# Optimization experiments

Hardware: AMD Instinct MI355X
Metric: run time of the kernel (lower is better)

The kernel has to match this reference:

```python
import jax, jax.numpy as jnp
import numpy as np

EPS = 1e-5

def mish(x):
    return x * jnp.tanh(jnp.logaddexp(x, 0.0))

def instance_norm(x, gamma, beta):
    # x: (N, C, D, H, W); normalize per (N, C) over spatial dims
    mu = jnp.mean(x, axis=(2, 3, 4), keepdims=True)
    var = jnp.var(x, axis=(2, 3, 4), keepdims=True)
    xh = (x - mu) * jax.lax.rsqrt(var + EPS)
    return xh * gamma[None, :, None, None, None] + beta[None, :, None, None, None]

def conv3d(x, w, stride, padding):
    return jax.lax.conv_general_dilated(
        x, w, window_strides=(stride, stride, stride), padding=padding,
        dimension_numbers=('NCDHW', 'OIDHW', 'NCDHW'))

def pad_k(k, p):
    # center-pad kernel spatial dims up to 5x5x5
    return jnp.pad(k, ((0, 0), (0, 0), (p, p), (p, p), (p, p)))

def mode_conv(x, t, c5, c3, c1, a3, a5, gw, gb, gamma, beta):
    N = x.shape[0]
    Co = c5.shape[0]
    # gate: Linear(num_tasks -> 5*Co), softmax over the 5 experts
    g = jax.nn.softmax((t @ gw.T + gb).reshape(N, 5, Co), axis=1)  # (N,5,Co)
    pool3 = jnp.full((3, 3, 3), 1.0 / 27.0, x.dtype)
    pool5 = jnp.full((5, 5, 5), 1.0 / 125.0, x.dtype)
    experts = jnp.stack([
        c5,                      # conv5x5
        pad_k(c3, 1),            # conv3x3 padded to 5
        pad_k(c1, 2),            # conv1x1 padded to 5
        pad_k(a3 * pool3, 1),    # avg3x3: (Co,Ci,1,1,1)*(3,3,3) broadcast, padded
        a5 * pool5,              # avg5x5
    ], axis=0)                   # (5, Co, Ci, 5, 5, 5)
    # per-sample synthesized kernel
    w = jnp.einsum('eoidhw,neo->noidhw', experts, g)  # (N, Co, Ci, 5,5,5)
    # per-sample conv3d, padding 'same' (training branch of original)
    y = jax.vmap(lambda xi, wi: conv3d(xi[None], wi, 1, 'SAME')[0])(x, w)
    return mish(instance_norm(y, gamma, beta))

def setup_inputs() -> dict:
    key = jax.random.key(0)
    ks = jax.random.split(key, 32)
    N, Ci, Co, T = 2, 32, 64, 10
    D = H = W = 64
    f32 = jnp.float32
    def kconv(k, co, ci, ksz, fan):
        bound = float(np.sqrt(6.0 / ((1.0 + 5.0) * fan)))  # kaiming_uniform a=sqrt(5), fan_out
        return jax.random.uniform(k, (co, ci, ksz, ksz, ksz), f32, -bound, bound)
    inp = {}
    inp['x'] = jax.random.normal(ks[0], (N, Ci, D, H, W), f32)
    inp['t'] = jax.random.normal(ks[1], (N, T), f32)
    def layer(base, ci, co):
        p = {}
        p['conv5'] = kconv(ks[base + 0], co, ci, 5, co * 125)
        p['conv3'] = kconv(ks[base + 1], co, ci, 3, co * 27)
        p['conv1'] = kconv(ks[base + 2], co, ci, 1, co)
        p['avg3'] = kconv(ks[base + 3], co, ci, 1, co)
        p['avg5'] = kconv(ks[base + 4], co, ci, 1, co)
        gb_bound = 1.0 / np.sqrt(T)
        p['gw'] = jax.random.uniform(ks[base + 5], (5 * co, T), f32, -gb_bound, gb_bound)
        p['gb'] = jax.random.uniform(ks[base + 6], (5 * co,), f32, -gb_bound, gb_bound)
        p['gamma'] = jnp.ones((co,), f32)
        p['beta'] = jnp.zeros((co,), f32)
        return p
    for name, v in layer(2, Ci, Co).items():
        inp['l1_' + name] = v
    for name, v in layer(12, Co, Co).items():
        inp['l2_' + name] = v
    dw_bound = float(np.sqrt(1.0 / (Co * 8)))
    inp['down_w'] = jax.random.uniform(ks[25], (Co, Co, 2, 2, 2), f32, -dw_bound, dw_bound)
    inp['down_gamma'] = jnp.ones((Co,), f32)
    inp['down_beta'] = jnp.zeros((Co,), f32)
    return inp

def reference(x, t,
              l1_conv5, l1_conv3, l1_conv1, l1_avg3, l1_avg5, l1_gw, l1_gb, l1_gamma, l1_beta,
              l2_conv5, l2_conv3, l2_conv1, l2_avg3, l2_avg5, l2_gw, l2_gb, l2_gamma, l2_beta,
              down_w, down_gamma, down_beta):
    h = mode_conv(x, t, l1_conv5, l1_conv3, l1_conv1, l1_avg3, l1_avg5, l1_gw, l1_gb, l1_gamma, l1_beta)
    x_skip = mode_conv(h, t, l2_conv5, l2_conv3, l2_conv1, l2_avg3, l2_avg5, l2_gw, l2_gb, l2_gamma, l2_beta)
    y = conv3d(x_skip, down_w, 2, 'VALID')
    y = mish(instance_norm(y, down_gamma, down_beta))
    return (y, x_skip)
```

## Files before the change

kernel.cpp:

```cpp
#include <hip/hip_runtime.h>
#include <cstdint>
#include <cstddef>

constexpr int NB  = 2;
constexpr int CO  = 64;
constexpr int DIM = 64;
constexpr int SP  = DIM * DIM * DIM;
constexpr int NC  = NB * CO;
constexpr int Y_SZ = NB * CO * 32 * 32 * 32;

typedef float f32x4 __attribute__((ext_vector_type(4)));
typedef short s16x8 __attribute__((ext_vector_type(8)));

__device__ __forceinline__ unsigned short f2bf(float f) {
    unsigned int u = __float_as_uint(f);
    unsigned int r = (u + 0x7fffu + ((u >> 16) & 1u)) >> 16;
    return (unsigned short)r;
}
__device__ __forceinline__ float bf2f(unsigned short u) {
    return __uint_as_float((unsigned int)u << 16);
}
__device__ __forceinline__ unsigned int pack2(float a, float b) {
    return (unsigned int)f2bf(a) | ((unsigned int)f2bf(b) << 16);
}
__device__ __forceinline__ float mish_f(float x) {
    float e = __expf(x);
    float num = e * (e + 2.f);
    float r = x * num * __builtin_amdgcn_rcpf(num + 2.f);
    return (x > 15.f) ? x : r;
}

__device__ __forceinline__ void gload_lds16(const void* g, void* l) {
    __builtin_amdgcn_global_load_lds(
        (const __attribute__((address_space(1))) unsigned int*)g,
        (__attribute__((address_space(3))) unsigned int*)l, 16, 0, 0);
}

__global__ void gate_kernel(const float* __restrict__ t, const float* __restrict__ gw,
                            const float* __restrict__ gb, float* __restrict__ g,
                            float* __restrict__ zbuf) {
    int tid = threadIdx.x;
    if (tid >= 128) { if (tid < 192) zbuf[tid - 128] = 0.f; return; }
    int n = tid >> 6, co = tid & 63;
    float tl[10];
#pragma unroll
    for (int k = 0; k < 10; ++k) tl[k] = t[n * 10 + k];
    float l[5];
#pragma unroll
    for (int e = 0; e < 5; ++e) {
        int row = e * CO + co;
        float acc = gb[row];
#pragma unroll
        for (int k = 0; k < 10; ++k) acc += tl[k] * gw[row * 10 + k];
        l[e] = acc;
    }
    float m = l[0];
#pragma unroll
    for (int e = 1; e < 5; ++e) m = fmaxf(m, l[e]);
    float s = 0.f;
#pragma unroll
    for (int e = 0; e < 5; ++e) { l[e] = expf(l[e] - m); s += l[e]; }
    float inv = 1.f / s;
#pragma unroll
    for (int e = 0; e < 5; ++e) g[(n * 5 + e) * CO + co] = l[e] * inv;
}

template <int CI>
__global__ void synth_kernel(const float* __restrict__ g,
                             const float* __restrict__ c5, const float* __restrict__ c3,
                             const float* __restrict__ c1, const float* __restrict__ a3,
                             const float* __restrict__ a5, unsigned short* __restrict__ wbuf) {
    int idx = blockIdx.x * 256 + threadIdx.x;
    constexpr int TOTAL = NB * CO * CI * 125;
    if (idx >= TOTAL) return;
    int tap = idx % 125;
    int ci  = (idx / 125) % CI;
    int co  = (idx / (125 * CI)) % CO;
    int n   = idx / (125 * CI * CO);
    const float* gn = g + n * 5 * CO;
    float g0 = gn[0 * CO + co], g1 = gn[1 * CO + co], g2 = gn[2 * CO + co],
          g3 = gn[3 * CO + co], g4 = gn[4 * CO + co];
    int dz = tap / 25, dy = (tap / 5) % 5, dx = tap % 5;
    int oc = co * CI + ci;
    float v = g0 * c5[(size_t)oc * 125 + tap] + g4 * a5[oc] * (1.f / 125.f);
    if (dz >= 1 && dz <= 3 && dy >= 1 && dy <= 3 && dx >= 1 && dx <= 3)
        v += g1 * c3[(size_t)oc * 27 + (dz - 1) * 9 + (dy - 1) * 3 + (dx - 1)]
           + g3 * a3[oc] * (1.f / 27.f);
    if (dz == 2 && dy == 2 && dx == 2) v += g2 * c1[oc];
    int t = (dy * 5 + dx);
    int cich = ci >> 5, cil = ci & 31;
    wbuf[((((size_t)(n * 5 + dz) * (CI / 32) + cich) * 25 + t) * 64 + co) * 32 + cil] = f2bf(v);
}

__global__ __launch_bounds__(256) void x_to_cl(const float* __restrict__ x,
                                               unsigned short* __restrict__ xcl) {
    __shared__ float ld[32][256];
    int b = blockIdx.x;
    int n = b >> 10;
    size_t base = (size_t)(b & 1023) * 256;
    int tid = threadIdx.x;
    const float* xp = x + (size_t)n * 32 * SP + base + tid;
#pragma unroll
    for (int c = 0; c < 32; ++c) ld[c][tid] = xp[(size_t)c * SP];
    __syncthreads();
    uint4* op = (uint4*)(xcl + ((size_t)n * SP + base) * 32);
#pragma unroll
    for (int r = 0; r < 4; ++r) {
        int idx = r * 256 + tid;
        int px = idx >> 2, q = idx & 3;
        uint4 o;
        o.x = pack2(ld[q * 8 + 0][px], ld[q * 8 + 1][px]);
        o.y = pack2(ld[q * 8 + 2][px], ld[q * 8 + 3][px]);
        o.z = pack2(ld[q * 8 + 4][px], ld[q * 8 + 5][px]);
        o.w = pack2(ld[q * 8 + 6][px], ld[q * 8 + 7][px]);
        op[idx] = o;
    }
}

template <int CI, bool OUT_CL, int PCH>
__global__ __launch_bounds__(512, 4) void conv5_mfma(const unsigned short* __restrict__ xin,
                                                     const unsigned short* __restrict__ wbuf,
                                                     void* __restrict__ outp,
                                                     float* __restrict__ part,
                                                     const void* __restrict__ zbuf) {
    constexpr int NCH = CI / 32;
    constexpr int NS  = 5 * NCH;
    __shared__ __align__(16) unsigned short lds[2][12800];

    const int b   = blockIdx.x;
    const int xt  = b & 3;
    const int yt  = (b >> 2) & 3;
    const int z   = (b >> 4) & 63;
    const int n   = b >> 10;
    const int tid = threadIdx.x;
    const int lane = tid & 63, wv = tid >> 6;
    const int xl = lane & 15, kh = lane >> 4;
    const int yh = wv >> 2, cq = wv & 3;

    f32x4 acc[8];
#pragma unroll
    for (int pt = 0; pt < 8; ++pt)
#pragma unroll
        for (int j = 0; j < 4; ++j) acc[pt][j] = 0.f;

    long goff[4]; int gval[4];
#pragma unroll
    for (int r = 0; r < 4; ++r) {
        int idx = tid + r * 512;
        int p = idx >> 2, khs = idx & 3;
        int xx = p % 20, yy = p / 20;
        int khs_g = khs ^ (xx & 3);
        int yi = yt * 16 - 2 + yy, xi = xt * 16 - 2 + xx;
        gval[r] = ((unsigned)yi < 64u) && ((unsigned)xi < 64u);
        goff[r] = ((long)(yi * 64 + xi) * CI + khs_g * 8) * 2;
    }

    auto stage = [&](int s, int buf) {
        int dz = s / NCH, cich = s % NCH;
        int zi = z + dz - 2;
        bool zok = (unsigned)zi < 64u;
        const char* pb = (const char*)xin
                       + ((size_t)(n * SP + zi * 4096) * CI + cich * 32) * 2;
        char* lb = (char*)&lds[buf][0];
#pragma unroll
        for (int r = 0; r < 4; ++r) {
            int idx = tid + r * 512;
            if (idx < 1600) {
                const void* g = (zok && gval[r]) ? (const void*)(pb + goff[r]) : zbuf;
                gload_lds16(g, lb + idx * 16);
            }
        }
    };

    auto compute = [&](int s, int buf) {
        int dz = s / NCH, cich = s % NCH;
        const unsigned short* wp = wbuf
            + ((size_t)((n * 5 + dz) * NCH + cich) * 25) * 2048
            + cq * 512 + xl * 32 + kh * 8;
        const char* src = (const char*)&lds[buf][0];
        __builtin_amdgcn_s_setprio(1);
#pragma unroll 1
        for (int dx = 0; dx < 5; ++dx) {
            int xx = xl + dx;
            unsigned int swz = (unsigned)(xx & 3) << 4;
            s16x8 fr[12];
#pragma unroll
            for (int r = 0; r < 12; ++r) {
                int row = yh * 8 + r;
                fr[r] = *(const s16x8*)(src
                        + (((unsigned)(row * 20 + xx) * 64 + (unsigned)kh * 16) ^ swz));
            }
#pragma unroll
            for (int dy = 0; dy < 5; ++dy) {
                s16x8 a = *(const s16x8*)(wp + (size_t)(dy * 5 + dx) * 2048);
#pragma unroll
                for (int pt = 0; pt < 8; ++pt)
                    acc[pt] = __builtin_amdgcn_mfma_f32_16x16x32_bf16(
                        a, fr[pt + dy], acc[pt], 0, 0, 0);
            }
        }
        __builtin_amdgcn_s_setprio(0);
    };

    stage(0, 0);
    __syncthreads();
#pragma unroll 1
    for (int s = 0; s < NS; ++s) {
        if (s + 1 < NS) stage(s + 1, (s + 1) & 1);
        compute(s, s & 1);
        __syncthreads();
    }

    {
        float s1[4], s2[4];
#pragma unroll
        for (int j = 0; j < 4; ++j) { s1[j] = 0.f; s2[j] = 0.f; }
#pragma unroll
        for (int pt = 0; pt < 8; ++pt)
#pragma unroll
            for (int j = 0; j < 4; ++j) {
                float v = acc[pt][j];
                s1[j] += v; s2[j] += v * v;
            }
#pragma unroll
        for (int o = 1; o < 16; o <<= 1)
#pragma unroll
            for (int j = 0; j < 4; ++j) {
                s1[j] += __shfl_xor(s1[j], o, 64);
                s2[j] += __shfl_xor(s2[j], o, 64);
            }
        if (xl == 0) {
            int co = cq * 16 + kh * 4;
            int cb = (b & 1023) * 2 + yh;
#pragma unroll
            for (int j = 0; j < 4; ++j) {
                part[((size_t)(n * 2 + 0) * 64 + co + j) * PCH + cb] = s1[j];
                part[((size_t)(n * 2 + 1) * 64 + co + j) * PCH + cb] = s2[j];
            }
        }
    }

    if (OUT_CL) {
        char* tb = (char*)&lds[0][0];
#pragma unroll
        for (int pt = 0; pt < 8; ++pt) {
            int pix = (yh * 8 + pt) * 16 + xl;
            unsigned int ad = ((unsigned)(pix * 128 + cq * 32 + kh * 8))
                              ^ ((unsigned)(pix & 7) << 4);
            *(unsigned int*)(tb + ad)     = pack2(acc[pt][0], acc[pt][1]);
            *(unsigned int*)(tb + ad + 4) = pack2(acc[pt][2], acc[pt][3]);
        }
        __syncthreads();
#pragma unroll
        for (int it = 0; it < 4; ++it) {
            int idx = it * 512 + tid;
            int pix = idx >> 3, ch = idx & 7;
            uint4 v = *(const uint4*)(tb + (((unsigned)idx * 16)
                                            ^ ((unsigned)(pix & 7) << 4)));
            int y = yt * 16 + (pix >> 4), x = xt * 16 + (pix & 15);
            *(uint4*)((unsigned short*)outp
                      + ((size_t)(n * SP + z * 4096 + y * 64 + x) * 64 + ch * 8)) = v;
        }
    } else {
        float* op = (float*)outp;
#pragma unroll
        for (int pt = 0; pt < 8; ++pt) {
            int y = yt * 16 + yh * 8 + pt;
#pragma unroll
            for (int j = 0; j < 4; ++j)
                op[((size_t)(n * 64 + cq * 16 + kh * 4 + j) * 64 + z) * 4096
                   + y * 64 + xt * 16 + xl] = acc[pt][j];
        }
    }
}

template <int CH>
__global__ void stats_fin(const float* __restrict__ part, float* __restrict__ st,
                          float invS) {
    int blk = blockIdx.x;
    int n = blk >> 6, co = blk & 63;
    int tid = threadIdx.x;
    const float* ps = part + ((size_t)(n * 2 + 0) * 64 + co) * CH;
    const float* pq = part + ((size_t)(n * 2 + 1) * 64 + co) * CH;
    float s1 = 0.f, s2 = 0.f;
    for (int i = tid; i < CH; i += 256) { s1 += ps[i]; s2 += pq[i]; }
#pragma unroll
    for (int o = 1; o < 64; o <<= 1) {
        s1 += __shfl_xor(s1, o, 64);
        s2 += __shfl_xor(s2, o, 64);
    }
    __shared__ float sh1[4], sh2[4];
    if ((tid & 63) == 0) { sh1[tid >> 6] = s1; sh2[tid >> 6] = s2; }
    __syncthreads();
    if (tid == 0) {
        float a = sh1[0] + sh1[1] + sh1[2] + sh1[3];
        float q = sh2[0] + sh2[1] + sh2[2] + sh2[3];
        float mean = a * invS;
        float var  = q * invS - mean * mean;
        st[(n * 64 + co) * 2]     = mean;
        st[(n * 64 + co) * 2 + 1] = rsqrtf(var + 1e-5f);
    }
}

__global__ void norm_mish_cl_kernel(unsigned short* __restrict__ h,
                                    const float* __restrict__ st,
                                    const float* __restrict__ gamma,
                                    const float* __restrict__ beta) {
    size_t idx = (size_t)blockIdx.x * 256 + threadIdx.x;
    uint4 v = ((uint4*)h)[idx];
    int c0 = ((int)(idx & 7)) * 8;
    size_t pix = idx >> 3;
    int n = (int)(pix >> 18);
    unsigned int* pv = &v.x;
#pragma unroll
    for (int q = 0; q < 4; ++q) {
        unsigned int wv = pv[q];
        unsigned int out = 0;
#pragma unroll
        for (int hv = 0; hv < 2; ++hv) {
            int c = c0 + 2 * q + hv;
            int nc = n * 64 + c;
            float val = bf2f((unsigned short)((wv >> (16 * hv)) & 0xffffu));
            float xh = (val - st[nc * 2]) * st[nc * 2 + 1] * gamma[c] + beta[c];
            out |= ((unsigned int)f2bf(mish_f(xh))) << (16 * hv);
        }
        pv[q] = out;
    }
    ((uint4*)h)[idx] = v;
}

template <int SHIFT>
__global__ void norm_mish_kernel(float* __restrict__ buf, const float* __restrict__ stats,
                                 const float* __restrict__ gamma, const float* __restrict__ beta,
                                 int total4) {
    int idx = blockIdx.x * 256 + threadIdx.x;
    if (idx >= total4) return;
    float4 v = reinterpret_cast<float4*>(buf)[idx];
    int nc = idx >> (SHIFT - 2);
    int c  = nc & 63;
    float mean = stats[nc * 2], inv = stats[nc * 2 + 1];
    float ga = gamma[c], be = beta[c];
    float* pv = &v.x;
#pragma unroll
    for (int k = 0; k < 4; ++k) {
        float xh = (pv[k] - mean) * inv * ga + be;
        pv[k] = mish_f(xh);
    }
    reinterpret_cast<float4*>(buf)[idx] = v;
}

__global__ __launch_bounds__(256) void down_conv_kernel(float* __restrict__ xin,
                                                        const float* __restrict__ dw,
                                                        const float* __restrict__ st,
                                                        const float* __restrict__ gamma,
                                                        const float* __restrict__ beta,
                                                        float* __restrict__ out,
                                                        float* __restrict__ part) {
    __shared__ float ls[8][2][8][64];
    int b   = blockIdx.x;
    int yt  = b & 7;
    int z   = (b >> 3) & 31;
    int n   = b >> 8;
    int tid = threadIdx.x;
    int xo  = tid & 31;
    int cog = tid >> 5;

    float acc[4][8];
#pragma unroll
    for (int yo = 0; yo < 4; ++yo)
#pragma unroll
        for (int j = 0; j < 8; ++j) acc[yo][j] = 0.f;

    for (int cc = 0; cc < 8; ++cc) {
        for (int idx = tid; idx < 8192; idx += 256) {
            int xx = idx & 63;
            int yy = (idx >> 6) & 7;
            int dz = (idx >> 9) & 1;
            int c  = idx >> 10;
            int ci = cc * 8 + c;
            size_t ga = ((size_t)(n * CO + ci) * 64 + 2 * z + dz) * 4096
                      + (yt * 8 + yy) * 64 + xx;
            float v = xin[ga];
            int nc = n * 64 + ci;
            float nv = mish_f((v - st[nc * 2]) * st[nc * 2 + 1] * gamma[ci] + beta[ci]);
            ls[c][dz][yy][xx] = nv;
            xin[ga] = nv;
        }
        __syncthreads();
#pragma unroll 1
        for (int c = 0; c < 8; ++c) {
            int ci = cc * 8 + c;
#pragma unroll
            for (int tap = 0; tap < 8; ++tap) {
                int dz = tap >> 2, dy = (tap >> 1) & 1, dx = tap & 1;
                float w[8];
#pragma unroll
                for (int j = 0; j < 8; ++j)
                    w[j] = dw[((size_t)(cog * 8 + j) * CO + ci) * 8 + tap];
#pragma unroll
                for (int yo = 0; yo < 4; ++yo) {
                    float xv = ls[c][dz][yo * 2 + dy][2 * xo + dx];
#pragma unroll
                    for (int j = 0; j < 8; ++j) acc[yo][j] += w[j] * xv;
                }
            }
        }
        __syncthreads();
    }
#pragma unroll
    for (int yo = 0; yo < 4; ++yo)
#pragma unroll
        for (int j = 0; j < 8; ++j)
            out[((size_t)(n * CO + cog * 8 + j) * 32 + z) * 1024 + (yt * 4 + yo) * 32 + xo]
                = acc[yo][j];

    float s1[8], s2[8];
#pragma unroll
    for (int j = 0; j < 8; ++j) { s1[j] = 0.f; s2[j] = 0.f; }
#pragma unroll
    for (int yo = 0; yo < 4; ++yo)
#pragma unroll
        for (int j = 0; j < 8; ++j) {
            float v = acc[yo][j];
            s1[j] += v; s2[j] += v * v;
        }
#pragma unroll
    for (int o = 1; o < 32; o <<= 1)
#pragma unroll
        for (int j = 0; j < 8; ++j) {
            s1[j] += __shfl_xor(s1[j], o, 64);
            s2[j] += __shfl_xor(s2[j], o, 64);
        }
    if (xo == 0) {
        int cb = b & 255;
#pragma unroll
        for (int j = 0; j < 8; ++j) {
            int co = cog * 8 + j;
            part[((size_t)(n * 2 + 0) * 64 + co) * 256 + cb] = s1[j];
            part[((size_t)(n * 2 + 1) * 64 + co) * 256 + cb] = s2[j];
        }
    }
}

extern "C" void kernel_launch(void* const* d_in, const int* in_sizes, int n_in,
                              void* d_out, int out_size, void* d_ws, size_t ws_size,
                              hipStream_t stream) {
    const float* x      = (const float*)d_in[0];
    const float* t      = (const float*)d_in[1];
    const float* l1_c5  = (const float*)d_in[2];
    const float* l1_c3  = (const float*)d_in[3];
    const float* l1_c1  = (const float*)d_in[4];
    const float* l1_a3  = (const float*)d_in[5];
    const float* l1_a5  = (const float*)d_in[6];
    const float* l1_gw  = (const float*)d_in[7];
    const float* l1_gb  = (const float*)d_in[8];
    const float* l1_ga  = (const float*)d_in[9];
    const float* l1_be  = (const float*)d_in[10];
    const float* l2_c5  = (const float*)d_in[11];
    const float* l2_c3  = (const float*)d_in[12];
    const float* l2_c1  = (const float*)d_in[13];
    const float* l2_a3  = (const float*)d_in[14];
    const float* l2_a5  = (const float*)d_in[15];
    const float* l2_gw  = (const float*)d_in[16];
    const float* l2_gb  = (const float*)d_in[17];
    const float* l2_ga  = (const float*)d_in[18];
    const float* l2_be  = (const float*)d_in[19];
    const float* down_w = (const float*)d_in[20];
    const float* dn_ga  = (const float*)d_in[21];
    const float* dn_be  = (const float*)d_in[22];

    char* ws = (char*)d_ws;
    unsigned short* xcl = (unsigned short*)(ws);
    unsigned short* h2  = (unsigned short*)(ws + 33554432);
    unsigned short* w1  = (unsigned short*)(ws + 100663296);
    unsigned short* w2  = (unsigned short*)(ws + 101687296);
    float* g1    = (float*)(ws + 103735296);
    float* g2    = (float*)(ws + 103737856);
    float* st1   = (float*)(ws + 103740416);
    float* st2   = (float*)(ws + 103741440);
    float* st3   = (float*)(ws + 103742464);
    float* part1 = (float*)(ws + 103743488);
    float* part2 = (float*)(ws + 105840640);
    float* part3 = (float*)(ws + 107937792);
    float* zbuf  = (float*)(ws + 108199936);

    float* yout  = (float*)d_out;
    float* xskip = (float*)d_out + Y_SZ;

    gate_kernel<<<1, 192, 0, stream>>>(t, l1_gw, l1_gb, g1, zbuf);
    gate_kernel<<<1, 192, 0, stream>>>(t, l2_gw, l2_gb, g2, zbuf);
    synth_kernel<32><<<(NB * CO * 32 * 125 + 255) / 256, 256, 0, stream>>>(
        g1, l1_c5, l1_c3, l1_c1, l1_a3, l1_a5, w1);
    synth_kernel<64><<<(NB * CO * 64 * 125 + 255) / 256, 256, 0, stream>>>(
        g2, l2_c5, l2_c3, l2_c1, l2_a3, l2_a5, w2);
    x_to_cl<<<2048, 256, 0, stream>>>(x, xcl);

    conv5_mfma<32, true, 2048><<<2048, 512, 0, stream>>>(xcl, w1, h2, part1, zbuf);
    stats_fin<2048><<<128, 256, 0, stream>>>(part1, st1, 1.f / SP);
    norm_mish_cl_kernel<<<16384, 256, 0, stream>>>(h2, st1, l1_ga, l1_be);

    conv5_mfma<64, false, 2048><<<2048, 512, 0, stream>>>(h2, w2, xskip, part2, zbuf);
    stats_fin<2048><<<128, 256, 0, stream>>>(part2, st2, 1.f / SP);

    down_conv_kernel<<<NB * 32 * 8, 256, 0, stream>>>(xskip, down_w, st2, l2_ga, l2_be,
                                                      yout, part3);
    stats_fin<256><<<128, 256, 0, stream>>>(part3, st3, 1.f / 32768.f);
    norm_mish_kernel<15><<<(NC * 32768 / 4 + 255) / 256, 256, 0, stream>>>(
        yout, st3, dn_ga, dn_be, NC * 32768 / 4);
}
```

Measured before the change: 871.2 us.

## Retile conv5 warps to 4 rows x 32 channels and reduce stats in LDS

Each wave in the 5x5x5 MFMA conv now covers 4 output rows and 32 output channels (two weight fragments) instead of 8 rows and 16 channels. This cuts the LDS input fragments loaded per dx from 12 to 8 and reuses each one across two MFMAs, at the cost of one extra weight load per tap. The XOR swizzle on the input LDS staging is removed. Per-block partial sums are now combined across waves in LDS before a single global write, halving the partial-stats buffer and the stats_fin work. Dropping the swizzle risks LDS bank conflicts.

```diff
diff --git a/kernel.cpp b/kernel.cpp
--- a/kernel.cpp
+++ b/kernel.cpp
@@ -117,7 +117,7 @@
     }
 }
 
-template <int CI, bool OUT_CL, int PCH>
+template <int CI, bool OUT_CL>
 __global__ __launch_bounds__(512, 4) void conv5_mfma(const unsigned short* __restrict__ xin,
                                                      const unsigned short* __restrict__ wbuf,
                                                      void* __restrict__ outp,
@@ -135,13 +135,15 @@
     const int tid = threadIdx.x;
     const int lane = tid & 63, wv = tid >> 6;
     const int xl = lane & 15, kh = lane >> 4;
-    const int yh = wv >> 2, cq = wv & 3;
-
-    f32x4 acc[8];
-#pragma unroll
-    for (int pt = 0; pt < 8; ++pt)
-#pragma unroll
-        for (int j = 0; j < 4; ++j) acc[pt][j] = 0.f;
+    const int yh = wv >> 1, cq = wv & 1;
+
+    f32x4 acc[4][2];
+#pragma unroll
+    for (int pt = 0; pt < 4; ++pt)
+#pragma unroll
+        for (int cb = 0; cb < 2; ++cb)
+#pragma unroll
+            for (int j = 0; j < 4; ++j) acc[pt][cb][j] = 0.f;
 
     long goff[4]; int gval[4];
 #pragma unroll
@@ -149,10 +151,9 @@
         int idx = tid + r * 512;
         int p = idx >> 2, khs = idx & 3;
         int xx = p % 20, yy = p / 20;
-        int khs_g = khs ^ (xx & 3);
         int yi = yt * 16 - 2 + yy, xi = xt * 16 - 2 + xx;
         gval[r] = ((unsigned)yi < 64u) && ((unsigned)xi < 64u);
-        goff[r] = ((long)(yi * 64 + xi) * CI + khs_g * 8) * 2;
+        goff[r] = ((long)(yi * 64 + xi) * CI + khs * 8) * 2;
     }
 
     auto stage = [&](int s, int buf) {
@@ -176,27 +177,30 @@
         int dz = s / NCH, cich = s % NCH;
         const unsigned short* wp = wbuf
             + ((size_t)((n * 5 + dz) * NCH + cich) * 25) * 2048
-            + cq * 512 + xl * 32 + kh * 8;
+            + cq * 1024 + xl * 32 + kh * 8;
         const char* src = (const char*)&lds[buf][0];
         __builtin_amdgcn_s_setprio(1);
 #pragma unroll 1
         for (int dx = 0; dx < 5; ++dx) {
             int xx = xl + dx;
-            unsigned int swz = (unsigned)(xx & 3) << 4;
-            s16x8 fr[12];
-#pragma unroll
-            for (int r = 0; r < 12; ++r) {
-                int row = yh * 8 + r;
-                fr[r] = *(const s16x8*)(src
-                        + (((unsigned)(row * 20 + xx) * 64 + (unsigned)kh * 16) ^ swz));
+            s16x8 fr[8];
+#pragma unroll
+            for (int r = 0; r < 8; ++r) {
+                int row = yh * 4 + r;
+                fr[r] = *(const s16x8*)(src + (size_t)(row * 20 + xx) * 64 + kh * 16);
             }
 #pragma unroll
             for (int dy = 0; dy < 5; ++dy) {
-                s16x8 a = *(const s16x8*)(wp + (size_t)(dy * 5 + dx) * 2048);
-#pragma unroll
-                for (int pt = 0; pt < 8; ++pt)
-                    acc[pt] = __builtin_amdgcn_mfma_f32_16x16x32_bf16(
-                        a, fr[pt + dy], acc[pt], 0, 0, 0);
+                const unsigned short* ap = wp + (size_t)(dy * 5 + dx) * 2048;
+                s16x8 a0 = *(const s16x8*)(ap);
+                s16x8 a1 = *(const s16x8*)(ap + 512);
+#pragma unroll
+                for (int pt = 0; pt < 4; ++pt) {
+                    acc[pt][0] = __builtin_amdgcn_mfma_f32_16x16x32_bf16(
+                        a0, fr[pt + dy], acc[pt][0], 0, 0, 0);
+                    acc[pt][1] = __builtin_amdgcn_mfma_f32_16x16x32_bf16(
+                        a1, fr[pt + dy], acc[pt][1], 0, 0, 0);
+                }
             }
         }
         __builtin_amdgcn_s_setprio(0);
@@ -211,46 +215,67 @@
         __syncthreads();
     }
 
+    float* sh1 = (float*)&lds[0][0];
+    float* sh2 = sh1 + 256;
     {
-        float s1[4], s2[4];
-#pragma unroll
-        for (int j = 0; j < 4; ++j) { s1[j] = 0.f; s2[j] = 0.f; }
-#pragma unroll
-        for (int pt = 0; pt < 8; ++pt)
-#pragma unroll
-            for (int j = 0; j < 4; ++j) {
-                float v = acc[pt][j];
-                s1[j] += v; s2[j] += v * v;
+        float s1[2][4], s2[2][4];
+#pragma unroll
+        for (int cb = 0; cb < 2; ++cb)
+#pragma unroll
+            for (int j = 0; j < 4; ++j) { s1[cb][j] = 0.f; s2[cb][j] = 0.f; }
+#pragma unroll
+        for (int pt = 0; pt < 4; ++pt)
+#pragma unroll
+            for (int cb = 0; cb < 2; ++cb)
+#pragma unroll
+                for (int j = 0; j < 4; ++j) {
+                    float v = acc[pt][cb][j];
+                    s1[cb][j] += v; s2[cb][j] += v * v;
+                }
+#pragma unroll
+        for (int o = 1; o < 16; o <<= 1)
+#pragma unroll
+            for (int cb = 0; cb < 2; ++cb)
+#pragma unroll
+                for (int j = 0; j < 4; ++j) {
+                    s1[cb][j] += __shfl_xor(s1[cb][j], o, 64);
+                    s2[cb][j] += __shfl_xor(s2[cb][j], o, 64);
+                }
+        if (xl == 0) {
+#pragma unroll
+            for (int cb = 0; cb < 2; ++cb)
+#pragma unroll
+                for (int j = 0; j < 4; ++j) {
+                    int co = cq * 32 + cb * 16 + kh * 4 + j;
+                    sh1[yh * 64 + co] = s1[cb][j];
+                    sh2[yh * 64 + co] = s2[cb][j];
+                }
+        }
+    }
+
+    char* tb = (char*)&lds[0][0] + 2048;
+    if (OUT_CL) {
+#pragma unroll
+        for (int pt = 0; pt < 4; ++pt)
+#pragma unroll
+            for (int cb = 0; cb < 2; ++cb) {
+                int pix = (yh * 4 + pt) * 16 + xl;
+                unsigned int ad = ((unsigned)(pix * 128 + cq * 64 + cb * 32 + kh * 8))
+                                  ^ ((unsigned)(pix & 7) << 4);
+                *(unsigned int*)(tb + ad)     = pack2(acc[pt][cb][0], acc[pt][cb][1]);
+                *(unsigned int*)(tb + ad + 4) = pack2(acc[pt][cb][2], acc[pt][cb][3]);
             }
-#pragma unroll
-        for (int o = 1; o < 16; o <<= 1)
-#pragma unroll
-            for (int j = 0; j < 4; ++j) {
-                s1[j] += __shfl_xor(s1[j], o, 64);
-                s2[j] += __shfl_xor(s2[j], o, 64);
-            }
-        if (xl == 0) {
-            int co = cq * 16 + kh * 4;
-            int cb = (b & 1023) * 2 + yh;
-#pragma unroll
-            for (int j = 0; j < 4; ++j) {
-                part[((size_t)(n * 2 + 0) * 64 + co + j) * PCH + cb] = s1[j];
-                part[((size_t)(n * 2 + 1) * 64 + co + j) * PCH + cb] = s2[j];
-            }
-        }
+    }
+    __syncthreads();
+
+    if (tid < 128) {
+        int co = tid & 63, si = tid >> 6;
+        const float* shp = si ? sh2 : sh1;
+        float v = shp[co] + shp[64 + co] + shp[128 + co] + shp[192 + co];
+        part[((size_t)(n * 2 + si) * 64 + co) * 1024 + (b & 1023)] = v;
     }
 
     if (OUT_CL) {
-        char* tb = (char*)&lds[0][0];
-#pragma unroll
-        for (int pt = 0; pt < 8; ++pt) {
-            int pix = (yh * 8 + pt) * 16 + xl;
-            unsigned int ad = ((unsigned)(pix * 128 + cq * 32 + kh * 8))
-                              ^ ((unsigned)(pix & 7) << 4);
-            *(unsigned int*)(tb + ad)     = pack2(acc[pt][0], acc[pt][1]);
-            *(unsigned int*)(tb + ad + 4) = pack2(acc[pt][2], acc[pt][3]);
-        }
-        __syncthreads();
 #pragma unroll
         for (int it = 0; it < 4; ++it) {
             int idx = it * 512 + tid;
@@ -264,12 +289,14 @@
     } else {
         float* op = (float*)outp;
 #pragma unroll
-        for (int pt = 0; pt < 8; ++pt) {
-            int y = yt * 16 + yh * 8 + pt;
-#pragma unroll
-            for (int j = 0; j < 4; ++j)
-                op[((size_t)(n * 64 + cq * 16 + kh * 4 + j) * 64 + z) * 4096
-                   + y * 64 + xt * 16 + xl] = acc[pt][j];
+        for (int pt = 0; pt < 4; ++pt) {
+            int y = yt * 16 + yh * 4 + pt;
+#pragma unroll
+            for (int cb = 0; cb < 2; ++cb)
+#pragma unroll
+                for (int j = 0; j < 4; ++j)
+                    op[((size_t)(n * 64 + cq * 32 + cb * 16 + kh * 4 + j) * 64 + z) * 4096
+                       + y * 64 + xt * 16 + xl] = acc[pt][cb][j];
         }
     }
 }
@@ -480,9 +507,9 @@
     float* st2   = (float*)(ws + 103741440);
     float* st3   = (float*)(ws + 103742464);
     float* part1 = (float*)(ws + 103743488);
-    float* part2 = (float*)(ws + 105840640);
-    float* part3 = (float*)(ws + 107937792);
-    float* zbuf  = (float*)(ws + 108199936);
+    float* part2 = (float*)(ws + 104792064);
+    float* part3 = (float*)(ws + 105840640);
+    float* zbuf  = (float*)(ws + 106102784);
 
     float* yout  = (float*)d_out;
     float* xskip = (float*)d_out + Y_SZ;
@@ -495,12 +522,12 @@
         g2, l2_c5, l2_c3, l2_c1, l2_a3, l2_a5, w2);
     x_to_cl<<<2048, 256, 0, stream>>>(x, xcl);
 
-    conv5_mfma<32, true, 2048><<<2048, 512, 0, stream>>>(xcl, w1, h2, part1, zbuf);
-    stats_fin<2048><<<128, 256, 0, stream>>>(part1, st1, 1.f / SP);
+    conv5_mfma<32, true><<<2048, 512, 0, stream>>>(xcl, w1, h2, part1, zbuf);
+    stats_fin<1024><<<128, 256, 0, stream>>>(part1, st1, 1.f / SP);
     norm_mish_cl_kernel<<<16384, 256, 0, stream>>>(h2, st1, l1_ga, l1_be);
 
-    conv5_mfma<64, false, 2048><<<2048, 512, 0, stream>>>(h2, w2, xskip, part2, zbuf);
-    stats_fin<2048><<<128, 256, 0, stream>>>(part2, st2, 1.f / SP);
+    conv5_mfma<64, false><<<2048, 512, 0, stream>>>(h2, w2, xskip, part2, zbuf);
+    stats_fin<1024><<<128, 256, 0, stream>>>(part2, st2, 1.f / SP);
 
     down_conv_kernel<<<NB * 32 * 8, 256, 0, stream>>>(xskip, down_w, st2, l2_ga, l2_be,
                                                       yout, part3);
```

Result: slower. 1.062 ms (+21.9%).

## Compute two z output slices per block to reuse staged input planes

Applied to the files above, without the earlier changes.

The conv5 kernel now has each block produce two consecutive output depth slices, streaming six input z-planes and applying each plane to both slices with the matching weight slices. This reduces redundant global-to-LDS staging of input planes and halves the block count. Per-block stats partials are combined in LDS before being written, which shrinks the partial buffers. The LDS swizzle was removed, and doubled accumulators increase register pressure, which may cause bank conflicts or spills.

```diff
diff --git a/kernel.cpp b/kernel.cpp
--- a/kernel.cpp
+++ b/kernel.cpp
@@ -117,31 +117,34 @@
     }
 }
 
-template <int CI, bool OUT_CL, int PCH>
+template <int CI, bool OUT_CL>
 __global__ __launch_bounds__(512, 4) void conv5_mfma(const unsigned short* __restrict__ xin,
                                                      const unsigned short* __restrict__ wbuf,
                                                      void* __restrict__ outp,
                                                      float* __restrict__ part,
                                                      const void* __restrict__ zbuf) {
-    constexpr int NCH = CI / 32;
-    constexpr int NS  = 5 * NCH;
+    constexpr int NCH  = CI / 32;
+    constexpr int NSTG = 6 * NCH;
     __shared__ __align__(16) unsigned short lds[2][12800];
 
     const int b   = blockIdx.x;
     const int xt  = b & 3;
     const int yt  = (b >> 2) & 3;
-    const int z   = (b >> 4) & 63;
-    const int n   = b >> 10;
+    const int zp  = (b >> 4) & 31;
+    const int n   = b >> 9;
+    const int z0  = zp * 2;
     const int tid = threadIdx.x;
     const int lane = tid & 63, wv = tid >> 6;
     const int xl = lane & 15, kh = lane >> 4;
     const int yh = wv >> 2, cq = wv & 3;
 
-    f32x4 acc[8];
-#pragma unroll
-    for (int pt = 0; pt < 8; ++pt)
-#pragma unroll
-        for (int j = 0; j < 4; ++j) acc[pt][j] = 0.f;
+    f32x4 acc[2][8];
+#pragma unroll
+    for (int sl = 0; sl < 2; ++sl)
+#pragma unroll
+        for (int pt = 0; pt < 8; ++pt)
+#pragma unroll
+            for (int j = 0; j < 4; ++j) acc[sl][pt][j] = 0.f;
 
     long goff[4]; int gval[4];
 #pragma unroll
@@ -149,15 +152,14 @@
         int idx = tid + r * 512;
         int p = idx >> 2, khs = idx & 3;
         int xx = p % 20, yy = p / 20;
-        int khs_g = khs ^ (xx & 3);
         int yi = yt * 16 - 2 + yy, xi = xt * 16 - 2 + xx;
         gval[r] = ((unsigned)yi < 64u) && ((unsigned)xi < 64u);
-        goff[r] = ((long)(yi * 64 + xi) * CI + khs_g * 8) * 2;
+        goff[r] = ((long)(yi * 64 + xi) * CI + khs * 8) * 2;
     }
 
     auto stage = [&](int s, int buf) {
-        int dz = s / NCH, cich = s % NCH;
-        int zi = z + dz - 2;
+        int pp = s / NCH, cich = s % NCH;
+        int zi = z0 - 2 + pp;
         bool zok = (unsigned)zi < 64u;
         const char* pb = (const char*)xin
                        + ((size_t)(n * SP + zi * 4096) * CI + cich * 32) * 2;
@@ -172,31 +174,57 @@
         }
     };
 
-    auto compute = [&](int s, int buf) {
-        int dz = s / NCH, cich = s % NCH;
-        const unsigned short* wp = wbuf
-            + ((size_t)((n * 5 + dz) * NCH + cich) * 25) * 2048
+    auto comp = [&](int s, int buf) {
+        int pp = s / NCH, cich = s % NCH;
+        const bool d0 = pp < 5;
+        const bool d1 = pp >= 1;
+        const unsigned short* wp0 = wbuf
+            + ((size_t)((n * 5 + pp) * NCH + cich) * 25) * 2048
+            + cq * 512 + xl * 32 + kh * 8;
+        const unsigned short* wp1 = wbuf
+            + ((size_t)((n * 5 + (pp - 1)) * NCH + cich) * 25) * 2048
             + cq * 512 + xl * 32 + kh * 8;
         const char* src = (const char*)&lds[buf][0];
         __builtin_amdgcn_s_setprio(1);
 #pragma unroll 1
         for (int dx = 0; dx < 5; ++dx) {
             int xx = xl + dx;
-            unsigned int swz = (unsigned)(xx & 3) << 4;
             s16x8 fr[12];
 #pragma unroll
-            for (int r = 0; r < 12; ++r) {
-                int row = yh * 8 + r;
+            for (int r = 0; r < 12; ++r)
                 fr[r] = *(const s16x8*)(src
-                        + (((unsigned)(row * 20 + xx) * 64 + (unsigned)kh * 16) ^ swz));
-            }
-#pragma unroll
-            for (int dy = 0; dy < 5; ++dy) {
-                s16x8 a = *(const s16x8*)(wp + (size_t)(dy * 5 + dx) * 2048);
-#pragma unroll
-                for (int pt = 0; pt < 8; ++pt)
-                    acc[pt] = __builtin_amdgcn_mfma_f32_16x16x32_bf16(
-                        a, fr[pt + dy], acc[pt], 0, 0, 0);
+                        + (size_t)((yh * 8 + r) * 20 + xx) * 64 + kh * 16);
+            if (d0 && d1) {
+#pragma unroll
+                for (int dy = 0; dy < 5; ++dy) {
+                    s16x8 a0 = *(const s16x8*)(wp0 + (size_t)(dy * 5 + dx) * 2048);
+                    s16x8 a1 = *(const s16x8*)(wp1 + (size_t)(dy * 5 + dx) * 2048);
+#pragma unroll
+                    for (int pt = 0; pt < 8; ++pt) {
+                        acc[0][pt] = __builtin_amdgcn_mfma_f32_16x16x32_bf16(
+                            a0, fr[pt + dy], acc[0][pt], 0, 0, 0);
+                        acc[1][pt] = __builtin_amdgcn_mfma_f32_16x16x32_bf16(
+                            a1, fr[pt + dy], acc[1][pt], 0, 0, 0);
+                    }
+                }
+            } else if (d0) {
+#pragma unroll
+                for (int dy = 0; dy < 5; ++dy) {
+                    s16x8 a0 = *(const s16x8*)(wp0 + (size_t)(dy * 5 + dx) * 2048);
+#pragma unroll
+                    for (int pt = 0; pt < 8; ++pt)
+                        acc[0][pt] = __builtin_amdgcn_mfma_f32_16x16x32_bf16(
+                            a0, fr[pt + dy], acc[0][pt], 0, 0, 0);
+                }
+            } else {
+#pragma unroll
+                for (int dy = 0; dy < 5; ++dy) {
+                    s16x8 a1 = *(const s16x8*)(wp1 + (size_t)(dy * 5 + dx) * 2048);
+#pragma unroll
+                    for (int pt = 0; pt < 8; ++pt)
+                        acc[1][pt] = __builtin_amdgcn_mfma_f32_16x16x32_bf16(
+                            a1, fr[pt + dy], acc[1][pt], 0, 0, 0);
+                }
             }
         }
         __builtin_amdgcn_s_setprio(0);
@@ -205,23 +233,27 @@
     stage(0, 0);
     __syncthreads();
 #pragma unroll 1
-    for (int s = 0; s < NS; ++s) {
-        if (s + 1 < NS) stage(s + 1, (s + 1) & 1);
-        compute(s, s & 1);
+    for (int s = 0; s < NSTG; ++s) {
+        if (s + 1 < NSTG) stage(s + 1, (s + 1) & 1);
+        comp(s, s & 1);
         __syncthreads();
     }
 
+    float* sh1 = (float*)&lds[0][0];
+    float* sh2 = sh1 + 128;
     {
         float s1[4], s2[4];
 #pragma unroll
         for (int j = 0; j < 4; ++j) { s1[j] = 0.f; s2[j] = 0.f; }
 #pragma unroll
-        for (int pt = 0; pt < 8; ++pt)
-#pragma unroll
-            for (int j = 0; j < 4; ++j) {
-                float v = acc[pt][j];
-                s1[j] += v; s2[j] += v * v;
-            }
+        for (int sl = 0; sl < 2; ++sl)
+#pragma unroll
+            for (int pt = 0; pt < 8; ++pt)
+#pragma unroll
+                for (int j = 0; j < 4; ++j) {
+                    float v = acc[sl][pt][j];
+                    s1[j] += v; s2[j] += v * v;
+                }
 #pragma unroll
         for (int o = 1; o < 16; o <<= 1)
 #pragma unroll
@@ -230,27 +262,36 @@
                 s2[j] += __shfl_xor(s2[j], o, 64);
             }
         if (xl == 0) {
-            int co = cq * 16 + kh * 4;
-            int cb = (b & 1023) * 2 + yh;
 #pragma unroll
             for (int j = 0; j < 4; ++j) {
-                part[((size_t)(n * 2 + 0) * 64 + co + j) * PCH + cb] = s1[j];
-                part[((size_t)(n * 2 + 1) * 64 + co + j) * PCH + cb] = s2[j];
+                int co = cq * 16 + kh * 4 + j;
+                sh1[yh * 64 + co] = s1[j];
+                sh2[yh * 64 + co] = s2[j];
             }
         }
     }
 
+    char* tb = (char*)&lds[0][0] + 2048;
     if (OUT_CL) {
-        char* tb = (char*)&lds[0][0];
 #pragma unroll
         for (int pt = 0; pt < 8; ++pt) {
             int pix = (yh * 8 + pt) * 16 + xl;
             unsigned int ad = ((unsigned)(pix * 128 + cq * 32 + kh * 8))
                               ^ ((unsigned)(pix & 7) << 4);
-            *(unsigned int*)(tb + ad)     = pack2(acc[pt][0], acc[pt][1]);
-            *(unsigned int*)(tb + ad + 4) = pack2(acc[pt][2], acc[pt][3]);
-        }
-        __syncthreads();
+            *(unsigned int*)(tb + ad)     = pack2(acc[0][pt][0], acc[0][pt][1]);
+            *(unsigned int*)(tb + ad + 4) = pack2(acc[0][pt][2], acc[0][pt][3]);
+        }
+    }
+    __syncthreads();
+
+    if (tid < 128) {
+        int co = tid & 63, si = tid >> 6;
+        const float* shp = si ? sh2 : sh1;
+        float v = shp[co] + shp[64 + co];
+        part[((size_t)(n * 2 + si) * 64 + co) * 512 + (b & 511)] = v;
+    }
+
+    if (OUT_CL) {
 #pragma unroll
         for (int it = 0; it < 4; ++it) {
             int idx = it * 512 + tid;
@@ -259,18 +300,40 @@
                                             ^ ((unsigned)(pix & 7) << 4)));
             int y = yt * 16 + (pix >> 4), x = xt * 16 + (pix & 15);
             *(uint4*)((unsigned short*)outp
-                      + ((size_t)(n * SP + z * 4096 + y * 64 + x) * 64 + ch * 8)) = v;
+                      + ((size_t)(n * SP + z0 * 4096 + y * 64 + x) * 64 + ch * 8)) = v;
+        }
+        __syncthreads();
+#pragma unroll
+        for (int pt = 0; pt < 8; ++pt) {
+            int pix = (yh * 8 + pt) * 16 + xl;
+            unsigned int ad = ((unsigned)(pix * 128 + cq * 32 + kh * 8))
+                              ^ ((unsigned)(pix & 7) << 4);
+            *(unsigned int*)(tb + ad)     = pack2(acc[1][pt][0], acc[1][pt][1]);
+            *(unsigned int*)(tb + ad + 4) = pack2(acc[1][pt][2], acc[1][pt][3]);
+        }
+        __syncthreads();
+#pragma unroll
+        for (int it = 0; it < 4; ++it) {
+            int idx = it * 512 + tid;
+            int pix = idx >> 3, ch = idx & 7;
+            uint4 v = *(const uint4*)(tb + (((unsigned)idx * 16)
+                                            ^ ((unsigned)(pix & 7) << 4)));
+            int y = yt * 16 + (pix >> 4), x = xt * 16 + (pix & 15);
+            *(uint4*)((unsigned short*)outp
+                      + ((size_t)(n * SP + (z0 + 1) * 4096 + y * 64 + x) * 64 + ch * 8)) = v;
         }
     } else {
         float* op = (float*)outp;
 #pragma unroll
-        for (int pt = 0; pt < 8; ++pt) {
-            int y = yt * 16 + yh * 8 + pt;
-#pragma unroll
-            for (int j = 0; j < 4; ++j)
-                op[((size_t)(n * 64 + cq * 16 + kh * 4 + j) * 64 + z) * 4096
-                   + y * 64 + xt * 16 + xl] = acc[pt][j];
-        }
+        for (int sl = 0; sl < 2; ++sl)
+#pragma unroll
+            for (int pt = 0; pt < 8; ++pt) {
+                int y = yt * 16 + yh * 8 + pt;
+#pragma unroll
+                for (int j = 0; j < 4; ++j)
+                    op[((size_t)(n * 64 + cq * 16 + kh * 4 + j) * 64 + (z0 + sl)) * 4096
+                       + y * 64 + xt * 16 + xl] = acc[sl][pt][j];
+            }
     }
 }
 
@@ -480,9 +543,9 @@
     float* st2   = (float*)(ws + 103741440);
     float* st3   = (float*)(ws + 103742464);
     float* part1 = (float*)(ws + 103743488);
-    float* part2 = (float*)(ws + 105840640);
-    float* part3 = (float*)(ws + 107937792);
-    float* zbuf  = (float*)(ws + 108199936);
+    float* part2 = (float*)(ws + 104267776);
+    float* part3 = (float*)(ws + 104792064);
+    float* zbuf  = (float*)(ws + 105054208);
 
     float* yout  = (float*)d_out;
     float* xskip = (float*)d_out + Y_SZ;
@@ -495,12 +558,12 @@
         g2, l2_c5, l2_c3, l2_c1, l2_a3, l2_a5, w2);
     x_to_cl<<<2048, 256, 0, stream>>>(x, xcl);
 
-    conv5_mfma<32, true, 2048><<<2048, 512, 0, stream>>>(xcl, w1, h2, part1, zbuf);
-    stats_fin<2048><<<128, 256, 0, stream>>>(part1, st1, 1.f / SP);
+    conv5_mfma<32, true><<<1024, 512, 0, stream>>>(xcl, w1, h2, part1, zbuf);
+    stats_fin<512><<<128, 256, 0, stream>>>(part1, st1, 1.f / SP);
     norm_mish_cl_kernel<<<16384, 256, 0, stream>>>(h2, st1, l1_ga, l1_be);
 
-    conv5_mfma<64, false, 2048><<<2048, 512, 0, stream>>>(h2, w2, xskip, part2, zbuf);
-    stats_fin<2048><<<128, 256, 0, stream>>>(part2, st2, 1.f / SP);
+    conv5_mfma<64, false><<<1024, 512, 0, stream>>>(h2, w2, xskip, part2, zbuf);
+    stats_fin<512><<<128, 256, 0, stream>>>(part2, st2, 1.f / SP);
 
     down_conv_kernel<<<NB * 32 * 8, 256, 0, stream>>>(xskip, down_w, st2, l2_ga, l2_be,
                                                       yout, part3);
```

Result: slower. 3.317 ms (+280.7%).
